# Performance work log

Measured on AMD Instinct MI355X. Metric: run time of the kernel, lower is better.

Reference implementation:

```python
import jax, jax.numpy as jnp
import numpy as np

NEG_RATIO = 5          # neg_sample_ratio, also k (num_nodes-1 >> ratio)
THRESH = 0.7           # hard_neg_threshold
SMOOTH = 0.1           # label_smoothing
NUM_NODES = 200_000
DIM = 128
B = 1024               # batch size, all labels == 1 (all positives)
FILL_VAL = -1.0e9


def _l2_normalize(x, eps=1e-12):
    # F.normalize(p=2, dim=-1): divide by clamped L2 norm
    n = jnp.sqrt(jnp.sum(x * x, axis=-1, keepdims=True))
    return x / jnp.maximum(n, eps)


def setup_inputs() -> dict:
    key = jax.random.key(0)
    k1, k2, k3, k4 = jax.random.split(key, 4)
    src_nodes = jax.random.randint(k1, (B,), 0, NUM_NODES)
    dst_nodes = jax.random.randint(k2, (B,), 0, NUM_NODES)
    labels = jnp.ones((B,), dtype=jnp.float32)  # all positives -> pos_mask all True
    timestamps = jax.random.uniform(k3, (B,), dtype=jnp.float32)
    memory = jax.random.normal(k4, (NUM_NODES, DIM), dtype=jnp.float32)
    return {
        "src_nodes": src_nodes,
        "dst_nodes": dst_nodes,
        "labels": labels,
        "timestamps": timestamps,
        "memory": memory,
    }


def reference(src_nodes, dst_nodes, labels, timestamps, memory):
    # --- embedding gather + L2 normalize ---
    src_emb = memory[src_nodes]                      # [B, D]
    s = _l2_normalize(src_emb).astype(jnp.float16)   # use_half_precision=True
    c = _l2_normalize(memory).astype(jnp.float16)    # [N, D]

    # --- similarity [B, N], back to fp32 ---
    sim = jnp.matmul(s, c.T).astype(jnp.float32)

    # --- mask out ground-truth dst and below-threshold sims ---
    cols = jnp.arange(NUM_NODES)
    allowed = cols[None, :] != dst_nodes[:, None]    # exclude GT positives
    valid = allowed & (sim > THRESH)
    score = jnp.where(valid, sim, FILL_VAL)

    # --- top-k hard negatives per positive ---
    k = NEG_RATIO  # min(neg_sample_ratio, num_nodes-1)
    topk_vals, topk_idx = jax.lax.top_k(score, k)    # [B, k]
    is_real = (topk_vals > FILL_VAL + 1.0).reshape(-1)  # [B*k]

    # --- fallback random negatives (fixed-shape equivalent of the torch
    #     pack-real-then-pad-random assembly; total count == B*k either way) ---
    rkey = jax.random.key(42)
    rand_dst = jax.random.randint(rkey, (B * k,), 0, NUM_NODES)
    src_rep = jnp.repeat(src_nodes, k)               # [B*k]
    rand_dst = jnp.where(rand_dst == src_rep, (rand_dst + 1) % NUM_NODES, rand_dst)

    final_src = src_rep
    final_dst = jnp.where(is_real, topk_idx.reshape(-1), rand_dst)
    neg_ts = jnp.repeat(timestamps, k)

    # --- assemble augmented batch ---
    new_src = jnp.concatenate([src_nodes, final_src])
    new_dst = jnp.concatenate([dst_nodes, final_dst])
    new_labels = jnp.concatenate([labels, jnp.zeros((B * k,), labels.dtype)])
    new_ts = jnp.concatenate([timestamps, neg_ts])

    # --- label smoothing ---
    new_labels = new_labels * (1.0 - SMOOTH) + (1.0 - new_labels) * SMOOTH

    return new_src, new_dst, new_labels, new_ts, topk_vals
```

## Files before the change

### kernel.cpp

```cpp
#include <hip/hip_runtime.h>

#define NUM_NODES 200000
#define DIM 128
#define BATCH 1024
#define K_NEG 5
#define CAP 16
#define BN 256
#define THRESH 0.7f
#define FILL (-1.0e9f)

typedef __attribute__((ext_vector_type(8))) short short8;
typedef __attribute__((ext_vector_type(16))) float f32x16;

__device__ __forceinline__ unsigned short f2bf(float x) {
  unsigned u = __builtin_bit_cast(unsigned, x);
  return (unsigned short)((u + 0x7fffu + ((u >> 16) & 1u)) >> 16);
}

__device__ __forceinline__ void tf2x32(unsigned k0, unsigned k1,
                                       unsigned x0, unsigned x1,
                                       unsigned* o0, unsigned* o1) {
  unsigned ks2 = k0 ^ k1 ^ 0x1BD11BDAu;
  unsigned v0 = x0 + k0, v1 = x1 + k1;
#define TFR(r) { v0 += v1; v1 = (v1 << r) | (v1 >> (32 - r)); v1 ^= v0; }
  TFR(13) TFR(15) TFR(26) TFR(6)   v0 += k1;  v1 += ks2 + 1u;
  TFR(17) TFR(29) TFR(16) TFR(24)  v0 += ks2; v1 += k0 + 2u;
  TFR(13) TFR(15) TFR(26) TFR(6)   v0 += k0;  v1 += k1 + 3u;
  TFR(17) TFR(29) TFR(16) TFR(24)  v0 += k1;  v1 += ks2 + 4u;
  TFR(13) TFR(15) TFR(26) TFR(6)   v0 += ks2; v1 += k0 + 5u;
#undef TFR
  *o0 = v0; *o1 = v1;
}

__device__ __forceinline__ unsigned rbits32(unsigned ka, unsigned kb, unsigned m) {
  unsigned o0, o1;
  tf2x32(ka, kb, 0u, m, &o0, &o1);
  return o0 ^ o1;
}

__global__ void prep_kernel(const float* __restrict__ memory,
                            const int* __restrict__ src_nodes,
                            unsigned short* __restrict__ s16f,
                            int* __restrict__ cand_cnt) {
  int tid = threadIdx.x;
  int gid = blockIdx.x * 256 + tid;
  if (gid < BATCH) cand_cnt[gid] = 0;
  int row = blockIdx.x * 4 + (tid >> 6);
  int L = tid & 63;
  int s = src_nodes[row];
  float2 v = ((const float2*)(memory + (size_t)s * DIM))[L];
  float ss = v.x * v.x + v.y * v.y;
#pragma unroll
  for (int off = 32; off > 0; off >>= 1) ss += __shfl_xor(ss, off);
  float inv = 1.0f / fmaxf(sqrtf(ss), 1e-12f);
  unsigned p = (unsigned)f2bf(v.x * inv) | ((unsigned)f2bf(v.y * inv) << 16);
  int ms = row >> 5, l32 = row & 31;
  int c = L >> 2;
  int ks = c >> 1, half = c & 1;
  ((unsigned*)s16f)[(((ms * 8 + ks) * 64) + half * 32 + l32) * 4 + (L & 3)] = p;
}

__global__ __launch_bounds__(256, 2) void sim_scan_kernel(
    const float* __restrict__ memory,
    const unsigned short* __restrict__ s16f,
    const int* __restrict__ dst_nodes,
    int* __restrict__ cand_cnt,
    float* __restrict__ cand_val,
    int* __restrict__ cand_idx) {
  int tid = threadIdx.x;
  int wid = tid >> 6;
  int lane = tid & 63;
  int half = lane >> 5;
  int l32 = lane & 31;
  int jb = blockIdx.x * BN + wid * 64;

  short8 bf0[8], bf1[8];
#pragma unroll
  for (int js = 0; js < 2; ++js) {
    int j = jb + js * 32 + l32;
    bool jv = (j < NUM_NODES);
    const float4* rp4 = (const float4*)(memory + (size_t)j * DIM);
    float4 q[16];
#pragma unroll
    for (int ks = 0; ks < 8; ++ks) {
      q[ks * 2]     = jv ? rp4[ks * 4 + half * 2]     : make_float4(0.f, 0.f, 0.f, 0.f);
      q[ks * 2 + 1] = jv ? rp4[ks * 4 + half * 2 + 1] : make_float4(0.f, 0.f, 0.f, 0.f);
    }
    float ss = 0.0f;
#pragma unroll
    for (int i = 0; i < 16; ++i)
      ss += q[i].x * q[i].x + q[i].y * q[i].y + q[i].z * q[i].z + q[i].w * q[i].w;
    ss += __shfl_xor(ss, 32);
    float inv = 1.0f / fmaxf(sqrtf(ss), 1e-12f);
#pragma unroll
    for (int ks = 0; ks < 8; ++ks) {
      float4 a = q[ks * 2], b = q[ks * 2 + 1];
      short8 f;
      f[0] = (short)f2bf(a.x * inv); f[1] = (short)f2bf(a.y * inv);
      f[2] = (short)f2bf(a.z * inv); f[3] = (short)f2bf(a.w * inv);
      f[4] = (short)f2bf(b.x * inv); f[5] = (short)f2bf(b.y * inv);
      f[6] = (short)f2bf(b.z * inv); f[7] = (short)f2bf(b.w * inv);
      if (js == 0) bf0[ks] = f; else bf1[ks] = f;
    }
  }

  const short8* __restrict__ af = (const short8*)s16f;
  short8 acur[8], anext[8];
#pragma unroll
  for (int ks = 0; ks < 8; ++ks) acur[ks] = af[ks * 64 + lane];

  for (int ms = 0; ms < 32; ++ms) {
    if (ms < 31) {
#pragma unroll
      for (int ks = 0; ks < 8; ++ks) anext[ks] = af[((ms + 1) * 8 + ks) * 64 + lane];
    }
    f32x16 acc0, acc1;
#pragma unroll
    for (int i = 0; i < 16; ++i) { acc0[i] = 0.0f; acc1[i] = 0.0f; }
#pragma unroll
    for (int ks = 0; ks < 8; ++ks) {
      acc0 = __builtin_amdgcn_mfma_f32_32x32x16_bf16(acur[ks], bf0[ks], acc0, 0, 0, 0);
      acc1 = __builtin_amdgcn_mfma_f32_32x32x16_bf16(acur[ks], bf1[ks], acc1, 0, 0, 0);
    }
    float vm = acc0[0];
#pragma unroll
    for (int i = 1; i < 16; ++i) vm = fmaxf(vm, acc0[i]);
#pragma unroll
    for (int i = 0; i < 16; ++i) vm = fmaxf(vm, acc1[i]);
    if (vm > THRESH) {
#pragma unroll
      for (int js = 0; js < 2; ++js) {
        int gj = jb + js * 32 + l32;
#pragma unroll
        for (int r = 0; r < 16; ++r) {
          float v = (js == 0) ? acc0[r] : acc1[r];
          if (v > THRESH) {
            int gi = ms * 32 + (r & 3) + 8 * (r >> 2) + 4 * half;
            if (gj < NUM_NODES && gj != dst_nodes[gi]) {
              int p = atomicAdd(&cand_cnt[gi], 1);
              if (p < CAP) {
                cand_val[gi * CAP + p] = v;
                cand_idx[gi * CAP + p] = gj;
              }
            }
          }
        }
      }
    }
#pragma unroll
    for (int ks = 0; ks < 8; ++ks) acur[ks] = anext[ks];
  }
}

__global__ void finalize_kernel(const int* __restrict__ src_nodes,
                                const int* __restrict__ dst_nodes,
                                const float* __restrict__ labels,
                                const float* __restrict__ ts,
                                const int* __restrict__ cand_cnt,
                                const float* __restrict__ cand_val,
                                const int* __restrict__ cand_idx,
                                float* __restrict__ out) {
  int r = blockIdx.x * 256 + threadIdx.x;
  if (r >= BATCH) return;
  const int TOT = BATCH + BATCH * K_NEG;
  int srcv = src_nodes[r];
  float tsv = ts[r];
  out[r] = (float)srcv;
  out[TOT + r] = (float)dst_nodes[r];
  float l = labels[r];
  out[2 * TOT + r] = l * 0.9f + (1.0f - l) * 0.1f;
  out[3 * TOT + r] = tsv;

  int cnt = cand_cnt[r];
  cnt = cnt < CAP ? cnt : CAP;
  float cv[CAP]; int ci[CAP];
  for (int i = 0; i < cnt; ++i) { cv[i] = cand_val[r * CAP + i]; ci[i] = cand_idx[r * CAP + i]; }

  unsigned k1a, k1b, k2a, k2b;
  tf2x32(0u, 42u, 0u, 0u, &k1a, &k1b);
  tf2x32(0u, 42u, 0u, 1u, &k2a, &k2b);

  const unsigned span = 200000u;
  const unsigned mult = 167296u;

  for (int s = 0; s < K_NEG; ++s) {
    int sel = -1;
    for (int i = 0; i < cnt; ++i)
      if (sel < 0 || cv[i] > cv[sel] || (cv[i] == cv[sel] && ci[i] < ci[sel])) sel = i;
    float v = FILL; int idx = 0;
    if (sel >= 0) { v = cv[sel]; idx = ci[sel]; cv[sel] = FILL; ci[sel] = 0x7fffffff; }
    bool is_real = v > (FILL + 1.0f);

    unsigned m = (unsigned)(r * K_NEG + s);
    unsigned hi = rbits32(k1a, k1b, m);
    unsigned lo = rbits32(k2a, k2b, m);
    unsigned off = ((hi % span) * mult + (lo % span)) % span;
    int rd = (int)off;
    if (rd == srcv) rd = (rd + 1) % NUM_NODES;
    int fd = is_real ? idx : rd;

    int mi = (int)m;
    out[BATCH + mi] = (float)srcv;
    out[TOT + BATCH + mi] = (float)fd;
    out[2 * TOT + BATCH + mi] = 0.1f;
    out[3 * TOT + BATCH + mi] = tsv;
    out[4 * TOT + mi] = v;
  }
}

extern "C" void kernel_launch(void* const* d_in, const int* in_sizes, int n_in,
                              void* d_out, int out_size, void* d_ws, size_t ws_size,
                              hipStream_t stream) {
  const int* src = (const int*)d_in[0];
  const int* dst = (const int*)d_in[1];
  const float* labels = (const float*)d_in[2];
  const float* ts = (const float*)d_in[3];
  const float* memory = (const float*)d_in[4];
  float* out = (float*)d_out;

  char* ws = (char*)d_ws;
  unsigned short* s16f = (unsigned short*)ws;
  int* cand_cnt = (int*)(ws + 262144);
  float* cand_val = (float*)(ws + 266240);
  int* cand_idx = (int*)(ws + 331776);

  prep_kernel<<<256, 256, 0, stream>>>(memory, src, s16f, cand_cnt);
  int jblocks = (NUM_NODES + BN - 1) / BN;
  sim_scan_kernel<<<jblocks, 256, 0, stream>>>(memory, s16f, dst, cand_cnt, cand_val, cand_idx);
  finalize_kernel<<<(BATCH + 255) / 256, 256, 0, stream>>>(src, dst, labels, ts,
                                                           cand_cnt, cand_val, cand_idx, out);
}
```

Measured before the change: 209.8 us.

## Stage query fragments in shared memory instead of per-wave global loads

The sim-scan kernel now cooperatively loads the 256 KB bf16 query matrix in four 64 KB chunks into LDS. All four waves then read their A fragments from LDS, where before each wave streamed them from global/L2 with register double-buffering. The max reduction over accumulators also becomes a tree. This cuts redundant global traffic across waves but adds block-wide barriers and 64 KB of LDS per block, which limits occupancy and removes the prefetch overlap.

```diff
diff --git a/kernel.cpp b/kernel.cpp
--- a/kernel.cpp
+++ b/kernel.cpp
@@ -5,7 +5,8 @@
 #define BATCH 1024
 #define K_NEG 5
 #define CAP 16
-#define BN 256
+#define JW 64
+#define BN (4 * JW)
 #define THRESH 0.7f
 #define FILL (-1.0e9f)
 
@@ -67,14 +68,15 @@
     int* __restrict__ cand_cnt,
     float* __restrict__ cand_val,
     int* __restrict__ cand_idx) {
+  __shared__ short8 aT[4096];
   int tid = threadIdx.x;
   int wid = tid >> 6;
   int lane = tid & 63;
   int half = lane >> 5;
   int l32 = lane & 31;
-  int jb = blockIdx.x * BN + wid * 64;
-
-  short8 bf0[8], bf1[8];
+  int jb = blockIdx.x * BN + wid * JW;
+
+  short8 bf[2][8];
 #pragma unroll
   for (int js = 0; js < 2; ++js) {
     int j = jb + js * 32 + l32;
@@ -100,55 +102,64 @@
       f[2] = (short)f2bf(a.z * inv); f[3] = (short)f2bf(a.w * inv);
       f[4] = (short)f2bf(b.x * inv); f[5] = (short)f2bf(b.y * inv);
       f[6] = (short)f2bf(b.z * inv); f[7] = (short)f2bf(b.w * inv);
-      if (js == 0) bf0[ks] = f; else bf1[ks] = f;
+      bf[js][ks] = f;
     }
   }
 
-  const short8* __restrict__ af = (const short8*)s16f;
-  short8 acur[8], anext[8];
-#pragma unroll
-  for (int ks = 0; ks < 8; ++ks) acur[ks] = af[ks * 64 + lane];
-
-  for (int ms = 0; ms < 32; ++ms) {
-    if (ms < 31) {
-#pragma unroll
-      for (int ks = 0; ks < 8; ++ks) anext[ks] = af[((ms + 1) * 8 + ks) * 64 + lane];
-    }
-    f32x16 acc0, acc1;
-#pragma unroll
-    for (int i = 0; i < 16; ++i) { acc0[i] = 0.0f; acc1[i] = 0.0f; }
-#pragma unroll
-    for (int ks = 0; ks < 8; ++ks) {
-      acc0 = __builtin_amdgcn_mfma_f32_32x32x16_bf16(acur[ks], bf0[ks], acc0, 0, 0, 0);
-      acc1 = __builtin_amdgcn_mfma_f32_32x32x16_bf16(acur[ks], bf1[ks], acc1, 0, 0, 0);
-    }
-    float vm = acc0[0];
-#pragma unroll
-    for (int i = 1; i < 16; ++i) vm = fmaxf(vm, acc0[i]);
-#pragma unroll
-    for (int i = 0; i < 16; ++i) vm = fmaxf(vm, acc1[i]);
-    if (vm > THRESH) {
-#pragma unroll
-      for (int js = 0; js < 2; ++js) {
-        int gj = jb + js * 32 + l32;
-#pragma unroll
-        for (int r = 0; r < 16; ++r) {
-          float v = (js == 0) ? acc0[r] : acc1[r];
-          if (v > THRESH) {
-            int gi = ms * 32 + (r & 3) + 8 * (r >> 2) + 4 * half;
-            if (gj < NUM_NODES && gj != dst_nodes[gi]) {
-              int p = atomicAdd(&cand_cnt[gi], 1);
-              if (p < CAP) {
-                cand_val[gi * CAP + p] = v;
-                cand_idx[gi * CAP + p] = gj;
+  const short8* __restrict__ afg = (const short8*)s16f;
+
+  for (int p = 0; p < 4; ++p) {
+    __syncthreads();
+#pragma unroll
+    for (int c = 0; c < 16; ++c) {
+      int idx = c * 256 + tid;
+      aT[idx] = afg[p * 4096 + idx];
+    }
+    __syncthreads();
+
+#pragma unroll
+    for (int ml = 0; ml < 8; ++ml) {
+      int ms = p * 8 + ml;
+      short8 a[8];
+#pragma unroll
+      for (int ks = 0; ks < 8; ++ks) a[ks] = aT[(ml * 8 + ks) * 64 + lane];
+      f32x16 acc0, acc1;
+#pragma unroll
+      for (int i = 0; i < 16; ++i) { acc0[i] = 0.0f; acc1[i] = 0.0f; }
+#pragma unroll
+      for (int ks = 0; ks < 8; ++ks) {
+        acc0 = __builtin_amdgcn_mfma_f32_32x32x16_bf16(a[ks], bf[0][ks], acc0, 0, 0, 0);
+        acc1 = __builtin_amdgcn_mfma_f32_32x32x16_bf16(a[ks], bf[1][ks], acc1, 0, 0, 0);
+      }
+      float m[16];
+#pragma unroll
+      for (int i = 0; i < 16; ++i) m[i] = fmaxf(acc0[i], acc1[i]);
+#pragma unroll
+      for (int i = 0; i < 8; ++i) m[i] = fmaxf(m[i], m[i + 8]);
+#pragma unroll
+      for (int i = 0; i < 4; ++i) m[i] = fmaxf(m[i], m[i + 4]);
+      float vm = fmaxf(fmaxf(m[0], m[1]), fmaxf(m[2], m[3]));
+      if (vm > THRESH) {
+#pragma unroll
+        for (int js = 0; js < 2; ++js) {
+          int gj = jb + js * 32 + l32;
+#pragma unroll
+          for (int r = 0; r < 16; ++r) {
+            float v = (js == 0) ? acc0[r] : acc1[r];
+            if (v > THRESH) {
+              int gi = ms * 32 + (r & 3) + 8 * (r >> 2) + 4 * half;
+              if (gj < NUM_NODES && gj != dst_nodes[gi]) {
+                int pp = atomicAdd(&cand_cnt[gi], 1);
+                if (pp < CAP) {
+                  cand_val[gi * CAP + pp] = v;
+                  cand_idx[gi * CAP + pp] = gj;
+                }
               }
             }
           }
         }
       }
     }
-#pragma unroll
-    for (int ks = 0; ks < 8; ++ks) acur[ks] = anext[ks];
   }
 }
 
```

Result: slower. 229.2 us (+9.2%).
